# Kernel optimization log

Hardware: AMD Instinct MI355X
Metric: run time of the kernel (lower is better)

Reference implementation:

```python
import jax, jax.numpy as jnp
import numpy as np


def setup_inputs() -> dict:
    key = jax.random.key(0)
    ks = jax.random.split(key, 6)
    E, N, S = 6, 4096, 64
    std_b = (2.0 / (S + S)) ** 0.5
    std_a = (2.0 / (S + S)) ** 0.5
    return {
        "x": jax.random.normal(ks[0], (1, N, S), dtype=jnp.float32),
        "edge_matrix": jax.random.uniform(ks[1], (E, N, N), dtype=jnp.float32),
        "ba": jnp.zeros((S,), dtype=jnp.float32),
        "wz_wr_wh": jax.random.normal(ks[2], (E, S, 3 * S), dtype=jnp.float32) * std_b,
        "uz_ur": jax.random.normal(ks[3], (S, 2 * S), dtype=jnp.float32) * std_b,
        "uh": jax.random.normal(ks[4], (S, S), dtype=jnp.float32) * std_a,
        "iteration": 10,
    }


def reference(x, edge_matrix, ba, wz_wr_wh, uz_ur, uh, iteration):
    # x: [1, N, S]; edge_matrix: [E, N, N]; secondary_size == size branch.
    S = uh.shape[0]
    h = x[0]  # [N, S]

    def step(h, _):
        # activation[e] = edge_matrix[e]^T @ h + ba  -> [E, N, S]
        act = jnp.einsum('ejn,js->ens', edge_matrix, h) + ba
        # per-edge-type GRU projections, summed over edge types -> [N, 3S]
        zrh = jnp.einsum('ens,esk->nk', act, wz_wr_wh)
        wz, wr, wh = zrh[:, :S], zrh[:, S:2 * S], zrh[:, 2 * S:]
        uzr = h @ uz_ur  # [N, 2S]
        z = jax.nn.sigmoid(wz + uzr[:, :S])
        r = jax.nn.sigmoid(wr + uzr[:, S:])
        hh = jnp.tanh(wh + (r * h) @ uh)
        return (1.0 - z) * h + z * hh, None

    h, _ = jax.lax.scan(step, h, None, length=int(iteration))
    return h[None]  # [1, N, S]
```

## Files before the change

### kernel.cpp

```cpp
#include <hip/hip_runtime.h>
#include <cstdint>
#include <cstddef>

#define NN 4096
#define SS 64
#define EE 6
#define BN 64
#define KT 64
#define ITERS 10
#define NPAD 4160
#define NSG  128

typedef _Float16 f16x8 __attribute__((ext_vector_type(8)));
typedef float f32x4 __attribute__((ext_vector_type(4)));

__device__ __forceinline__ float sigf(float x) { return 1.0f / (1.0f + __expf(-x)); }

__device__ __forceinline__ size_t cb(int e, int wt, int sg, int q ) {
    return ((((size_t)e * (NN / 32) + wt) * NSG + sg) * 4 + q) * 512;
}

__global__ __launch_bounds__(256) void k_init(const float* __restrict__ x,
                                              float* __restrict__ h,
                                              _Float16* __restrict__ hTh,
                                              _Float16* __restrict__ hTl,
                                              int npad) {
    const int t = threadIdx.x;
    const int n = blockIdx.x * 16 + (t & 15);
    const int c0 = (t >> 4) * 4;
    float4 v = *(const float4*)(x + (size_t)n * SS + c0);
    *(float4*)(h + (size_t)n * SS + c0) = v;
    if (hTh) {
        const float vv[4] = {v.x, v.y, v.z, v.w};
#pragma unroll
        for (int k = 0; k < 4; k++) {
            _Float16 hi = (_Float16)vv[k];
            _Float16 lo = (_Float16)(vv[k] - (float)hi);
            hTh[(size_t)(c0 + k) * npad + n] = hi;
            hTl[(size_t)(c0 + k) * npad + n] = lo;
        }
    }
}

__global__ __launch_bounds__(256) void k_pack(const float* __restrict__ edge,
                                              _Float16* __restrict__ eTf) {
    __shared__ float tile[64][33];
    const int wt = blockIdx.x;
    const int sp = blockIdx.y;
    const int e  = blockIdx.z;
    const int n0 = wt * 32;
    const int j0 = sp * 64;
    const int t = threadIdx.x;
    {
        const int r = t >> 2;
        const int c = (t & 3) * 8;
        const float* src = edge + (size_t)e * NN * NN + (size_t)(j0 + r) * NN + n0 + c;
        float4 v0 = *(const float4*)(src);
        float4 v1 = *(const float4*)(src + 4);
        tile[r][c + 0] = v0.x; tile[r][c + 1] = v0.y; tile[r][c + 2] = v0.z; tile[r][c + 3] = v0.w;
        tile[r][c + 4] = v1.x; tile[r][c + 5] = v1.y; tile[r][c + 6] = v1.z; tile[r][c + 7] = v1.w;
    }
    __syncthreads();
    {
        const int lane = t & 63;
        const int q = t >> 6;
        const int sgl = q >> 1;
        const int nh = q & 1;
        const int ln = lane & 15;
        const int lk = (lane >> 4) * 8;
        f16x8 hi, lo;
#pragma unroll
        for (int i = 0; i < 8; i++) {
            const float v = tile[sgl * 32 + lk + i][nh * 16 + ln];
            _Float16 h = (_Float16)v;
            hi[i] = h;
            lo[i] = (_Float16)(v - (float)h);
        }
        const int sg = sp * 2 + sgl;
        *(f16x8*)(eTf + cb(e, wt, sg, nh * 2 + 0) + (size_t)lane * 8) = hi;
        *(f16x8*)(eTf + cb(e, wt, sg, nh * 2 + 1) + (size_t)lane * 8) = lo;
    }
}

__global__ __launch_bounds__(64, 4) void k_act4(const _Float16* __restrict__ eTf,
                                                const _Float16* __restrict__ hTh,
                                                const _Float16* __restrict__ hTl,
                                                float* __restrict__ act_part,
                                                int jtot) {
    const int wt = blockIdx.x;
    const int e  = blockIdx.y;
    const int js = blockIdx.z;
    const int lane = threadIdx.x;
    const int ln = lane & 15;
    const int lk = (lane >> 4) * 8;
    const int n0 = wt * 32;
    const int jbase = js * jtot;
    const int NSTEP = jtot / 32;
    const int sgbase = js * NSTEP;

    const _Float16* Abase = eTf + cb(e, wt, sgbase, 0) + (size_t)lane * 8;
    const size_t bbase = (size_t)ln * NPAD + jbase + lk;

    f32x4 acc[2][4];
#pragma unroll
    for (int nh = 0; nh < 2; nh++)
#pragma unroll
        for (int st = 0; st < 4; st++) acc[nh][st] = (f32x4)0.0f;

    f16x8 H0[2], L0[2], H1[2], L1[2];

#define LOADA(H, L, s_)                                                      \
    {                                                                        \
        const int sc = ((s_) < NSTEP) ? (s_) : 0;                            \
        const _Float16* p = Abase + (size_t)sc * 2048;                       \
        H[0] = *(const f16x8*)(p);                                           \
        L[0] = *(const f16x8*)(p + 512);                                     \
        H[1] = *(const f16x8*)(p + 1024);                                    \
        L[1] = *(const f16x8*)(p + 1536);                                    \
    }

#define COMPUTE(H, L, s)                                                     \
    {                                                                        \
        f16x8 bh[4], bl[4];                                                  \
        _Pragma("unroll")                                                    \
        for (int st = 0; st < 4; st++) {                                     \
            const size_t bo = bbase + (size_t)st * 16 * NPAD + (size_t)(s) * 32;\
            bh[st] = *(const f16x8*)(hTh + bo);                              \
            bl[st] = *(const f16x8*)(hTl + bo);                              \
        }                                                                    \
        _Pragma("unroll")                                                    \
        for (int nh = 0; nh < 2; nh++) {                                     \
            _Pragma("unroll")                                                \
            for (int st = 0; st < 4; st++) {                                 \
                acc[nh][st] = __builtin_amdgcn_mfma_f32_16x16x32_f16(        \
                    H[nh], bh[st], acc[nh][st], 0, 0, 0);                    \
                acc[nh][st] = __builtin_amdgcn_mfma_f32_16x16x32_f16(        \
                    H[nh], bl[st], acc[nh][st], 0, 0, 0);                    \
                acc[nh][st] = __builtin_amdgcn_mfma_f32_16x16x32_f16(        \
                    L[nh], bh[st], acc[nh][st], 0, 0, 0);                    \
            }                                                                \
        }                                                                    \
    }

    LOADA(H0, L0, 0);
    LOADA(H1, L1, 1);
    for (int s = 0; s < NSTEP; s += 2) {
        COMPUTE(H0, L0, s);     LOADA(H0, L0, s + 2);
        COMPUTE(H1, L1, s + 1); LOADA(H1, L1, s + 3);
    }
#undef LOADA
#undef COMPUTE

    float* ap = act_part + (size_t)(js * EE + e) * NN * SS;
#pragma unroll
    for (int nh = 0; nh < 2; nh++)
#pragma unroll
        for (int st = 0; st < 4; st++)
#pragma unroll
            for (int r = 0; r < 4; r++) {
                const int n = n0 + nh * 16 + (lane >> 4) * 4 + r;
                ap[(size_t)n * SS + st * 16 + ln] = acc[nh][st][r];
            }
}

__global__ __launch_bounds__(128, 4) void k_act_mfma(const float* __restrict__ edge,
                                                     const _Float16* __restrict__ hTh,
                                                     const _Float16* __restrict__ hTl,
                                                     float* __restrict__ act_part,
                                                     int jtot) {
    const int nt = blockIdx.x;
    const int e  = blockIdx.y;
    const int js = blockIdx.z;
    const int tid = threadIdx.x;
    const int w   = tid >> 6;
    const int lane = tid & 63;
    const int ln = lane & 15;
    const int lk = (lane >> 4) * 8;
    const int n0 = nt * 64 + w * 32;
    const int jbase = js * jtot;
    const int NSTEP = jtot / 32;

    const float* A0 = edge + (size_t)e * NN * NN + (size_t)(jbase + lk) * NN + (n0 + ln);
    const float* A1 = A0 + 16;
    const size_t bbase = (size_t)ln * NN + jbase + lk;

    f32x4 acc[2][4];
#pragma unroll
    for (int nh = 0; nh < 2; nh++)
#pragma unroll
        for (int st = 0; st < 4; st++) acc[nh][st] = (f32x4)0.0f;

    f16x8 h0[2], l0[2], h1[2], l1[2];

#define LOADA(H, L, s_)                                                      \
    {                                                                        \
        const int sc = ((s_) < NSTEP) ? (s_) : 0;                            \
        const size_t off = (size_t)sc * 32 * NN;                             \
        float t0[8], t1[8];                                                  \
        _Pragma("unroll")                                                    \
        for (int i = 0; i < 8; i++) {                                        \
            t0[i] = A0[off + (size_t)i * NN];                                \
            t1[i] = A1[off + (size_t)i * NN];                                \
        }                                                                    \
        _Pragma("unroll")                                                    \
        for (int i = 0; i < 8; i++) {                                        \
            _Float16 hi0 = (_Float16)t0[i];                                  \
            H[0][i] = hi0;                                                   \
            L[0][i] = (_Float16)(t0[i] - (float)hi0);                        \
            _Float16 hi1 = (_Float16)t1[i];                                  \
            H[1][i] = hi1;                                                   \
            L[1][i] = (_Float16)(t1[i] - (float)hi1);                        \
        }                                                                    \
    }

#define COMPUTE(H, L, s)                                                     \
    {                                                                        \
        f16x8 bh[4], bl[4];                                                  \
        _Pragma("unroll")                                                    \
        for (int st = 0; st < 4; st++) {                                     \
            const size_t bo = bbase + (size_t)st * 16 * NN + (size_t)(s) * 32;\
            bh[st] = *(const f16x8*)(hTh + bo);                              \
            bl[st] = *(const f16x8*)(hTl + bo);                              \
        }                                                                    \
        _Pragma("unroll")                                                    \
        for (int nh = 0; nh < 2; nh++) {                                     \
            _Pragma("unroll")                                                \
            for (int st = 0; st < 4; st++) {                                 \
                acc[nh][st] = __builtin_amdgcn_mfma_f32_16x16x32_f16(        \
                    H[nh], bh[st], acc[nh][st], 0, 0, 0);                    \
                acc[nh][st] = __builtin_amdgcn_mfma_f32_16x16x32_f16(        \
                    H[nh], bl[st], acc[nh][st], 0, 0, 0);                    \
                acc[nh][st] = __builtin_amdgcn_mfma_f32_16x16x32_f16(        \
                    L[nh], bh[st], acc[nh][st], 0, 0, 0);                    \
            }                                                                \
        }                                                                    \
    }

    LOADA(h0, l0, 0);
    LOADA(h1, l1, 1);
    for (int s = 0; s < NSTEP; s += 2) {
        COMPUTE(h0, l0, s);     LOADA(h0, l0, s + 2);
        COMPUTE(h1, l1, s + 1); LOADA(h1, l1, s + 3);
    }
#undef LOADA
#undef COMPUTE

    float* ap = act_part + (size_t)(js * EE + e) * NN * SS;
#pragma unroll
    for (int nh = 0; nh < 2; nh++)
#pragma unroll
        for (int st = 0; st < 4; st++)
#pragma unroll
            for (int r = 0; r < 4; r++) {
                const int n = n0 + nh * 16 + (lane >> 4) * 4 + r;
                ap[(size_t)n * SS + st * 16 + ln] = acc[nh][st][r];
            }
}

__global__ __launch_bounds__(128) void k_act(const float* __restrict__ edge,
                                             const float* __restrict__ h,
                                             float* __restrict__ act_part,
                                             int jtot) {
    __shared__ float hbuf[2][KT][SS];
    const int nb = blockIdx.x;
    const int e  = blockIdx.y;
    const int js = blockIdx.z;
    const int tid = threadIdx.x;
    const int ng = tid & 7;
    const int sg = tid >> 3;
    const int n0 = nb * BN;
    const int s0 = sg * 4;
    const int jbase = js * jtot;

    const float4* hsrc4 = (const float4*)(h + (size_t)jbase * SS);

    float acc[8][4];
#pragma unroll
    for (int i = 0; i < 8; i++)
#pragma unroll
        for (int k = 0; k < 4; k++) acc[i][k] = 0.0f;

    float4 pre[8];
#pragma unroll
    for (int r = 0; r < 8; r++) pre[r] = hsrc4[r * 128 + tid];
    {
        float4* dst = (float4*)&hbuf[0][0][0];
#pragma unroll
        for (int r = 0; r < 8; r++) dst[r * 128 + tid] = pre[r];
    }
    __syncthreads();

    const float* eg = edge + (size_t)e * NN * NN + (size_t)jbase * NN + n0 + ng * 8;

    float4 ea[4][2];
#pragma unroll
    for (int u = 0; u < 4; u++) {
        ea[u][0] = *(const float4*)(eg + (size_t)u * NN);
        ea[u][1] = *(const float4*)(eg + (size_t)u * NN + 4);
    }

    const int NCH = jtot / KT;
    for (int c = 0; c < NCH; c++) {
        if (c + 1 < NCH) {
#pragma unroll
            for (int r = 0; r < 8; r++) pre[r] = hsrc4[(c + 1) * (KT * SS / 4) + r * 128 + tid];
        }
        const float (*hb)[SS] = hbuf[c & 1];
        for (int jj = 0; jj < KT; jj += 4) {
            const int q = c * KT + jj + 4;
            const float* pe = eg + (size_t)(q < jtot ? q : 0) * NN;
            float4 eb[4][2];
#pragma unroll
            for (int u = 0; u < 4; u++) {
                eb[u][0] = *(const float4*)(pe + (size_t)u * NN);
                eb[u][1] = *(const float4*)(pe + (size_t)u * NN + 4);
            }
#pragma unroll
            for (int u = 0; u < 4; u++) {
                const float4 hv = *(const float4*)&hb[jj + u][s0];
                const float ev[8] = {ea[u][0].x, ea[u][0].y, ea[u][0].z, ea[u][0].w,
                                     ea[u][1].x, ea[u][1].y, ea[u][1].z, ea[u][1].w};
#pragma unroll
                for (int i = 0; i < 8; i++) {
                    acc[i][0] += ev[i] * hv.x;
                    acc[i][1] += ev[i] * hv.y;
                    acc[i][2] += ev[i] * hv.z;
                    acc[i][3] += ev[i] * hv.w;
                }
            }
#pragma unroll
            for (int u = 0; u < 4; u++) { ea[u][0] = eb[u][0]; ea[u][1] = eb[u][1]; }
        }
        if (c + 1 < NCH) {
            float4* dst = (float4*)&hbuf[(c + 1) & 1][0][0];
#pragma unroll
            for (int r = 0; r < 8; r++) dst[r * 128 + tid] = pre[r];
        }
        __syncthreads();
    }

    float* ap = act_part + (((size_t)js * EE + e) * NN + n0 + ng * 8) * SS + s0;
#pragma unroll
    for (int i = 0; i < 8; i++)
        *(float4*)(ap + (size_t)i * SS) = make_float4(acc[i][0], acc[i][1], acc[i][2], acc[i][3]);
}

__global__ __launch_bounds__(256) void k_update(const float* __restrict__ act_part,
                                                float* __restrict__ h,
                                                const float* __restrict__ W,
                                                const float* __restrict__ uz_ur,
                                                const float* __restrict__ uh,
                                                const float* __restrict__ ba,
                                                _Float16* __restrict__ hTh,
                                                _Float16* __restrict__ hTl,
                                                int jparts, int npad) {
    __shared__ float w_lds[SS][192];
    __shared__ float a_lds[16][68];
    __shared__ float h_lds[16][68];
    __shared__ float zrh_lds[16][196];
    __shared__ float uzr_lds[16][132];
    __shared__ float rh_lds[16][68];

    const int n0 = blockIdx.x * 16;
    const int t = threadIdx.x;
    const int nl = t & 15;
    const int kg = t >> 4;

    {
        const int row = t >> 4, c4 = t & 15;
        float4 v = *(const float4*)(h + (size_t)(n0 + row) * SS + c4 * 4);
        *(float4*)&h_lds[row][c4 * 4] = v;
    }

    float zacc[12];
#pragma unroll
    for (int k = 0; k < 12; k++) zacc[k] = 0.0f;
    const int k0 = kg * 12;

    for (int e = 0; e < EE; e++) {
        __syncthreads();
        {
            const float4* wsrc = (const float4*)(W + (size_t)e * SS * 192);
            float4* wdst = (float4*)&w_lds[0][0];
#pragma unroll
            for (int r = 0; r < 12; r++) wdst[r * 256 + t] = wsrc[r * 256 + t];
        }
        {
            const int row = t >> 4, c4 = t & 15;
            const size_t base = ((size_t)e * NN + (n0 + row)) * SS + c4 * 4;
            float4 bv = *(const float4*)(ba + c4 * 4);
            float vx = bv.x, vy = bv.y, vz = bv.z, vw = bv.w;
            for (int p = 0; p < jparts; p++) {
                float4 pp = *(const float4*)(act_part + base + (size_t)p * EE * NN * SS);
                vx += pp.x; vy += pp.y; vz += pp.z; vw += pp.w;
            }
            *(float4*)&a_lds[row][c4 * 4] = make_float4(vx, vy, vz, vw);
        }
        __syncthreads();
#pragma unroll 8
        for (int s = 0; s < SS; s++) {
            const float av = a_lds[nl][s];
            const float4* wrow = (const float4*)&w_lds[s][k0];
            const float4 w0 = wrow[0], w1 = wrow[1], w2 = wrow[2];
            zacc[0] += av * w0.x; zacc[1] += av * w0.y; zacc[2]  += av * w0.z; zacc[3]  += av * w0.w;
            zacc[4] += av * w1.x; zacc[5] += av * w1.y; zacc[6]  += av * w1.z; zacc[7]  += av * w1.w;
            zacc[8] += av * w2.x; zacc[9] += av * w2.y; zacc[10] += av * w2.z; zacc[11] += av * w2.w;
        }
    }

    float uacc[8];
#pragma unroll
    for (int k = 0; k < 8; k++) uacc[k] = 0.0f;
#pragma unroll 4
    for (int j = 0; j < SS; j++) {
        const float hv = h_lds[nl][j];
        const float4* urow = (const float4*)(uz_ur + (size_t)j * 128 + kg * 8);
        const float4 u0 = urow[0], u1 = urow[1];
        uacc[0] += hv * u0.x; uacc[1] += hv * u0.y; uacc[2] += hv * u0.z; uacc[3] += hv * u0.w;
        uacc[4] += hv * u1.x; uacc[5] += hv * u1.y; uacc[6] += hv * u1.z; uacc[7] += hv * u1.w;
    }

    *(float4*)&zrh_lds[nl][k0]     = make_float4(zacc[0], zacc[1], zacc[2], zacc[3]);
    *(float4*)&zrh_lds[nl][k0 + 4] = make_float4(zacc[4], zacc[5], zacc[6], zacc[7]);
    *(float4*)&zrh_lds[nl][k0 + 8] = make_float4(zacc[8], zacc[9], zacc[10], zacc[11]);
    *(float4*)&uzr_lds[nl][kg * 8]     = make_float4(uacc[0], uacc[1], uacc[2], uacc[3]);
    *(float4*)&uzr_lds[nl][kg * 8 + 4] = make_float4(uacc[4], uacc[5], uacc[6], uacc[7]);
    __syncthreads();

    const int sg4 = kg * 4;
    const float4 wz = *(const float4*)&zrh_lds[nl][sg4];
    const float4 wr = *(const float4*)&zrh_lds[nl][64 + sg4];
    const float4 wh = *(const float4*)&zrh_lds[nl][128 + sg4];
    const float4 uz = *(const float4*)&uzr_lds[nl][sg4];
    const float4 ur = *(const float4*)&uzr_lds[nl][64 + sg4];
    const float4 hv4 = *(const float4*)&h_lds[nl][sg4];

    float z4[4], rh4[4];
    {
        const float wzv[4] = {wz.x, wz.y, wz.z, wz.w};
        const float wrv[4] = {wr.x, wr.y, wr.z, wr.w};
        const float uzv[4] = {uz.x, uz.y, uz.z, uz.w};
        const float urv[4] = {ur.x, ur.y, ur.z, ur.w};
        const float hvv[4] = {hv4.x, hv4.y, hv4.z, hv4.w};
#pragma unroll
        for (int k = 0; k < 4; k++) {
            z4[k] = sigf(wzv[k] + uzv[k]);
            const float r = sigf(wrv[k] + urv[k]);
            rh4[k] = r * hvv[k];
        }
    }
    *(float4*)&rh_lds[nl][sg4] = make_float4(rh4[0], rh4[1], rh4[2], rh4[3]);
    __syncthreads();

    float hacc[4];
#pragma unroll
    for (int k = 0; k < 4; k++) hacc[k] = 0.0f;
#pragma unroll 4
    for (int j = 0; j < SS; j++) {
        const float rhv = rh_lds[nl][j];
        const float4 u = *(const float4*)(uh + (size_t)j * SS + sg4);
        hacc[0] += rhv * u.x; hacc[1] += rhv * u.y; hacc[2] += rhv * u.z; hacc[3] += rhv * u.w;
    }

    {
        const float whv[4] = {wh.x, wh.y, wh.z, wh.w};
        const float hvv[4] = {hv4.x, hv4.y, hv4.z, hv4.w};
        float ov[4];
#pragma unroll
        for (int k = 0; k < 4; k++) {
            const float hh = tanhf(whv[k] + hacc[k]);
            ov[k] = (1.0f - z4[k]) * hvv[k] + z4[k] * hh;
        }
        *(float4*)(h + (size_t)(n0 + nl) * SS + sg4) = make_float4(ov[0], ov[1], ov[2], ov[3]);
        if (hTh) {
#pragma unroll
            for (int k = 0; k < 4; k++) {
                _Float16 hi = (_Float16)ov[k];
                _Float16 lo = (_Float16)(ov[k] - (float)hi);
                hTh[(size_t)(sg4 + k) * npad + n0 + nl] = hi;
                hTl[(size_t)(sg4 + k) * npad + n0 + nl] = lo;
            }
        }
    }
}

extern "C" void kernel_launch(void* const* d_in, const int* in_sizes, int n_in,
                              void* d_out, int out_size, void* d_ws, size_t ws_size,
                              hipStream_t stream) {
    const float* x    = (const float*)d_in[0];
    const float* edge = (const float*)d_in[1];
    const float* ba   = (const float*)d_in[2];
    const float* W    = (const float*)d_in[3];
    const float* uzur = (const float*)d_in[4];
    const float* uh   = (const float*)d_in[5];

    float* h = (float*)d_out;
    char*  wsb = (char*)d_ws;

    const size_t actB = (size_t)EE * NN * SS * sizeof(float);
    const size_t hTB  = (size_t)SS * NPAD * sizeof(_Float16) * 2;
    const size_t hTBu = (size_t)SS * NN * sizeof(_Float16) * 2;
    const size_t eTfB = (size_t)EE * NN * NN * 2 * sizeof(_Float16);
    const int jp = 4;
    const size_t needFull = eTfB + (size_t)jp * actB + hTB;

    if (ws_size >= needFull) {
        _Float16* eTf = (_Float16*)wsb;
        float*    act = (float*)(wsb + eTfB);
        _Float16* hTh = (_Float16*)(wsb + eTfB + (size_t)jp * actB);
        _Float16* hTl = hTh + (size_t)SS * NPAD;
        const int jtot = NN / jp;

        k_init<<<NN / 16, 256, 0, stream>>>(x, h, hTh, hTl, NPAD);
        k_pack<<<dim3(NN / 32, NN / 64, EE), 256, 0, stream>>>(edge, eTf);

        for (int it = 0; it < ITERS; ++it) {
            k_act4<<<dim3(NN / 32, EE, jp), 64, 0, stream>>>(eTf, hTh, hTl, act, jtot);
            k_update<<<NN / 16, 256, 0, stream>>>(act, h, W, uzur, uh, ba, hTh, hTl, jp, NPAD);
        }
    } else {
        int jp2;
        bool use_mfma;
        if      (ws_size >= 4 * actB + hTBu) { jp2 = 4; use_mfma = true;  }
        else if (ws_size >= 2 * actB + hTBu) { jp2 = 2; use_mfma = true;  }
        else if (ws_size >= 1 * actB + hTBu) { jp2 = 1; use_mfma = true;  }
        else                                 { jp2 = 1; use_mfma = false; }

        float*     act = (float*)wsb;
        _Float16*  hTh = use_mfma ? (_Float16*)(wsb + (size_t)jp2 * actB) : nullptr;
        _Float16*  hTl = use_mfma ? (_Float16*)(wsb + (size_t)jp2 * actB) + (size_t)SS * NN : nullptr;
        const int jtot = NN / jp2;

        k_init<<<NN / 16, 256, 0, stream>>>(x, h, hTh, hTl, NN);
        for (int it = 0; it < ITERS; ++it) {
            if (use_mfma) {
                k_act_mfma<<<dim3(NN / 64, EE, jp2), 128, 0, stream>>>(edge, hTh, hTl, act, jtot);
            } else {
                k_act<<<dim3(NN / BN, EE, jp2), 128, 0, stream>>>(edge, h, act, jtot);
            }
            k_update<<<NN / 16, 256, 0, stream>>>(act, h, W, uzur, uh, ba, hTh, hTl, jp2, NN);
        }
    }
}
```

Before: 1.776 ms.

## Fuse edge-matrix packing into the first iteration's activation kernel

Replaces the standalone k_pack kernel with k_act_pack, which reads the fp32 edge matrix, splits it into fp16 hi/lo, writes the packed layout, and at the same time computes the first iteration's activation with MFMA. This removes one full extra read of the packed matrix in iteration 0, saving a pass over the large packed buffer. The trade-off is that the first iteration now does strided fp32 column reads without an LDS transpose, which may coalesce poorly.

```diff
diff --git a/kernel.cpp b/kernel.cpp
--- a/kernel.cpp
+++ b/kernel.cpp
@@ -42,44 +42,107 @@
     }
 }
 
-__global__ __launch_bounds__(256) void k_pack(const float* __restrict__ edge,
-                                              _Float16* __restrict__ eTf) {
-    __shared__ float tile[64][33];
-    const int wt = blockIdx.x;
-    const int sp = blockIdx.y;
-    const int e  = blockIdx.z;
+__global__ __launch_bounds__(128, 4) void k_act_pack(const float* __restrict__ edge,
+                                                     const _Float16* __restrict__ hTh,
+                                                     const _Float16* __restrict__ hTl,
+                                                     float* __restrict__ act_part,
+                                                     _Float16* __restrict__ eTf,
+                                                     int jtot) {
+    const int nt = blockIdx.x;
+    const int e  = blockIdx.y;
+    const int js = blockIdx.z;
+    const int tid = threadIdx.x;
+    const int w   = tid >> 6;
+    const int lane = tid & 63;
+    const int ln = lane & 15;
+    const int lk = (lane >> 4) * 8;
+    const int wt = nt * 2 + w;
     const int n0 = wt * 32;
-    const int j0 = sp * 64;
-    const int t = threadIdx.x;
-    {
-        const int r = t >> 2;
-        const int c = (t & 3) * 8;
-        const float* src = edge + (size_t)e * NN * NN + (size_t)(j0 + r) * NN + n0 + c;
-        float4 v0 = *(const float4*)(src);
-        float4 v1 = *(const float4*)(src + 4);
-        tile[r][c + 0] = v0.x; tile[r][c + 1] = v0.y; tile[r][c + 2] = v0.z; tile[r][c + 3] = v0.w;
-        tile[r][c + 4] = v1.x; tile[r][c + 5] = v1.y; tile[r][c + 6] = v1.z; tile[r][c + 7] = v1.w;
-    }
-    __syncthreads();
-    {
-        const int lane = t & 63;
-        const int q = t >> 6;
-        const int sgl = q >> 1;
-        const int nh = q & 1;
-        const int ln = lane & 15;
-        const int lk = (lane >> 4) * 8;
-        f16x8 hi, lo;
-#pragma unroll
-        for (int i = 0; i < 8; i++) {
-            const float v = tile[sgl * 32 + lk + i][nh * 16 + ln];
-            _Float16 h = (_Float16)v;
-            hi[i] = h;
-            lo[i] = (_Float16)(v - (float)h);
-        }
-        const int sg = sp * 2 + sgl;
-        *(f16x8*)(eTf + cb(e, wt, sg, nh * 2 + 0) + (size_t)lane * 8) = hi;
-        *(f16x8*)(eTf + cb(e, wt, sg, nh * 2 + 1) + (size_t)lane * 8) = lo;
-    }
+    const int jbase = js * jtot;
+    const int NSTEP = jtot / 32;
+    const int sgbase = js * NSTEP;
+
+    const float* A0 = edge + (size_t)e * NN * NN + (size_t)(jbase + lk) * NN + (n0 + ln);
+    const float* A1 = A0 + 16;
+    const size_t bbase = (size_t)ln * NPAD + jbase + lk;
+    _Float16* stbase = eTf + cb(e, wt, sgbase, 0) + (size_t)lane * 8;
+
+    f32x4 acc[2][4];
+#pragma unroll
+    for (int nh = 0; nh < 2; nh++)
+#pragma unroll
+        for (int st = 0; st < 4; st++) acc[nh][st] = (f32x4)0.0f;
+
+    f16x8 h0[2], l0[2], h1[2], l1[2];
+
+#define LOADA(H, L, s_)                                                      \
+    {                                                                        \
+        const int sc = ((s_) < NSTEP) ? (s_) : 0;                            \
+        const size_t off = (size_t)sc * 32 * NN;                             \
+        float t0[8], t1[8];                                                  \
+        _Pragma("unroll")                                                    \
+        for (int i = 0; i < 8; i++) {                                        \
+            t0[i] = A0[off + (size_t)i * NN];                                \
+            t1[i] = A1[off + (size_t)i * NN];                                \
+        }                                                                    \
+        _Pragma("unroll")                                                    \
+        for (int i = 0; i < 8; i++) {                                        \
+            _Float16 hi0 = (_Float16)t0[i];                                  \
+            H[0][i] = hi0;                                                   \
+            L[0][i] = (_Float16)(t0[i] - (float)hi0);                        \
+            _Float16 hi1 = (_Float16)t1[i];                                  \
+            H[1][i] = hi1;                                                   \
+            L[1][i] = (_Float16)(t1[i] - (float)hi1);                        \
+        }                                                                    \
+        _Float16* sp = stbase + (size_t)sc * 2048;                           \
+        *(f16x8*)(sp)        = H[0];                                         \
+        *(f16x8*)(sp + 512)  = L[0];                                         \
+        *(f16x8*)(sp + 1024) = H[1];                                         \
+        *(f16x8*)(sp + 1536) = L[1];                                         \
+    }
+
+#define COMPUTE(H, L, s)                                                     \
+    {                                                                        \
+        f16x8 bh[4], bl[4];                                                  \
+        _Pragma("unroll")                                                    \
+        for (int st = 0; st < 4; st++) {                                     \
+            const size_t bo = bbase + (size_t)st * 16 * NPAD + (size_t)(s) * 32;\
+            bh[st] = *(const f16x8*)(hTh + bo);                              \
+            bl[st] = *(const f16x8*)(hTl + bo);                              \
+        }                                                                    \
+        _Pragma("unroll")                                                    \
+        for (int nh = 0; nh < 2; nh++) {                                     \
+            _Pragma("unroll")                                                \
+            for (int st = 0; st < 4; st++) {                                 \
+                acc[nh][st] = __builtin_amdgcn_mfma_f32_16x16x32_f16(        \
+                    H[nh], bh[st], acc[nh][st], 0, 0, 0);                    \
+                acc[nh][st] = __builtin_amdgcn_mfma_f32_16x16x32_f16(        \
+                    H[nh], bl[st], acc[nh][st], 0, 0, 0);                    \
+                acc[nh][st] = __builtin_amdgcn_mfma_f32_16x16x32_f16(        \
+                    L[nh], bh[st], acc[nh][st], 0, 0, 0);                    \
+            }                                                                \
+        }                                                                    \
+    }
+
+    LOADA(h0, l0, 0);
+    LOADA(h1, l1, 1);
+    for (int s = 0; s < NSTEP; s += 2) {
+        COMPUTE(h0, l0, s);     LOADA(h0, l0, s + 2);
+        COMPUTE(h1, l1, s + 1); LOADA(h1, l1, s + 3);
+    }
+#undef LOADA
+#undef COMPUTE
+
+    float* ap = act_part + (size_t)(js * EE + e) * NN * SS;
+#pragma unroll
+    for (int nh = 0; nh < 2; nh++)
+#pragma unroll
+        for (int st = 0; st < 4; st++)
+#pragma unroll
+            for (int r = 0; r < 4; r++) {
+                const int n = n0 + nh * 16 + (lane >> 4) * 4 + r;
+                ap[(size_t)n * SS + st * 16 + ln] = acc[nh][st][r];
+            }
 }
 
 __global__ __launch_bounds__(64, 4) void k_act4(const _Float16* __restrict__ eTf,
@@ -512,9 +575,11 @@
         const int jtot = NN / jp;
 
         k_init<<<NN / 16, 256, 0, stream>>>(x, h, hTh, hTl, NPAD);
-        k_pack<<<dim3(NN / 32, NN / 64, EE), 256, 0, stream>>>(edge, eTf);
-
-        for (int it = 0; it < ITERS; ++it) {
+
+        k_act_pack<<<dim3(NN / 64, EE, jp), 128, 0, stream>>>(edge, hTh, hTl, act, eTf, jtot);
+        k_update<<<NN / 16, 256, 0, stream>>>(act, h, W, uzur, uh, ba, hTh, hTl, jp, NPAD);
+
+        for (int it = 1; it < ITERS; ++it) {
             k_act4<<<dim3(NN / 32, EE, jp), 64, 0, stream>>>(eTf, hTh, hTl, act, jtot);
             k_update<<<NN / 16, 256, 0, stream>>>(act, h, W, uzur, uh, ba, hTh, hTl, jp, NPAD);
         }
```

New measurement: 1.787 ms. About the same (+0.6%).
